# Kernel tuning notes

Measured on AMD Instinct MI355X. Metric: run time of the kernel, lower is better.

## Reference

```python
import jax, jax.numpy as jnp
import numpy as np

B_, L_, H_, D_, N_, R_, K_ = 2, 1024, 2048, 4096, 16, 128, 4


def setup_inputs() -> dict:
    key = jax.random.key(0)
    ks = jax.random.split(key, 8)
    s = lambda k, shp, sc: jax.random.normal(k, shp, jnp.float32) * sc
    x = s(ks[0], (B_, L_, H_), 1.0)
    in_proj_w = s(ks[1], (2 * D_, H_), 0.02)
    conv_w = s(ks[2], (D_, 1, K_), 0.1)          # depthwise conv kernel (OIW, I=1)
    conv_b = s(ks[3], (D_,), 0.02)
    x_proj_w = s(ks[4], (R_ + 2 * N_, D_), 0.02)
    dt_proj_w = s(ks[5], (D_, R_), 0.02)
    dt_proj_b = s(ks[6], (D_,), 0.02)
    # A_log init as in module: log(arange(1..N)) expanded over channels
    A_log = jnp.log(jnp.broadcast_to(jnp.arange(1, N_ + 1, dtype=jnp.float32), (D_, N_)))
    D = jnp.ones((D_,), jnp.float32)
    out_proj_w = s(ks[7], (H_, D_), 0.02)
    return dict(x=x, in_proj_w=in_proj_w, conv_w=conv_w, conv_b=conv_b,
                x_proj_w=x_proj_w, dt_proj_w=dt_proj_w, dt_proj_b=dt_proj_b,
                A_log=A_log, D=D, out_proj_w=out_proj_w)


def reference(x, in_proj_w, conv_w, conv_b, x_proj_w, dt_proj_w, dt_proj_b, A_log, D, out_proj_w):
    Bsz, L, H = x.shape
    # in_proj -> split into ssm branch and gate branch
    proj = x @ in_proj_w.T                               # [B, L, 2D]
    h, gate = jnp.split(proj, 2, axis=-1)                # each [B, L, D]
    # causal depthwise conv1d over time (left pad K-1, truncate to L)
    hc = h.transpose(0, 2, 1)                            # [B, D, L]
    conv = jax.lax.conv_general_dilated(
        hc, conv_w, window_strides=(1,), padding=[(K_ - 1, 0)],
        dimension_numbers=('NCW', 'OIW', 'NCW'), feature_group_count=hc.shape[1])
    u = jax.nn.silu(conv + conv_b[None, :, None]).transpose(0, 2, 1)  # [B, L, D]
    # input-dependent SSM parameters
    ssm_p = u @ x_proj_w.T                               # [B, L, R+2N]
    dt, Bm, Cm = jnp.split(ssm_p, [R_, R_ + N_], axis=-1)
    dt = jax.nn.softplus(dt @ dt_proj_w.T + dt_proj_b)   # [B, L, D]
    A = -jnp.exp(A_log)                                  # [D, N]

    def step(state, inp):
        dt_t, B_t, C_t, u_t = inp                        # [B,D],[B,N],[B,N],[B,D]
        dA = jnp.exp(dt_t[:, :, None] * A)               # [B, D, N]
        dBu = dt_t[:, :, None] * B_t[:, None, :] * u_t[:, :, None]
        state = state * dA + dBu                         # [B, D, N]
        y = jnp.einsum('bdn,bn->bd', state, C_t)
        return state, y

    init = jnp.zeros((Bsz, u.shape[-1], N_), x.dtype)
    _, ys = jax.lax.scan(step, init, (dt.transpose(1, 0, 2), Bm.transpose(1, 0, 2),
                                      Cm.transpose(1, 0, 2), u.transpose(1, 0, 2)))
    y = ys.transpose(1, 0, 2)                            # [B, L, D]
    y = (y + u * D) * jax.nn.silu(gate)
    return y @ out_proj_w.T                              # [B, L, H]
```

## Files before the change

### kernel.cpp

```cpp
#include <hip/hip_runtime.h>
#include <hip/hip_bf16.h>
#include <cstdint>
#include <cstddef>

typedef __hip_bfloat16 bf16;
typedef __attribute__((ext_vector_type(8))) short short8;
typedef __attribute__((ext_vector_type(4))) float f32x4;

#define BB 2
#define LL 1024
#define HH 2048
#define DD 4096
#define NN 16
#define RR 128
#define KK 4
#define TT (BB*LL)
#define NC 16
#define LC (LL/NC)
#define KSPLIT 8

__device__ __forceinline__ void gload_lds16(const void* g, void* l) {
  __builtin_amdgcn_global_load_lds(
      (__attribute__((address_space(1))) void*)(g),
      (__attribute__((address_space(3))) void*)(l), 16, 0, 0);
}

__global__ void probe_dtype(const unsigned int* __restrict__ alog, int* __restrict__ flag) {
  if (threadIdx.x == 0 && blockIdx.x == 0) *flag = (alog[0] != 0u) ? 1 : 0;
}

__global__ __launch_bounds__(256) void cvt_bf16(
    const void* __restrict__ src, bf16* __restrict__ dst,
    int n4, const int* __restrict__ flag)
{
  const bool isb = (*flag != 0);
  const int stride = gridDim.x * blockDim.x;
  for (int i = blockIdx.x * blockDim.x + threadIdx.x; i < n4; i += stride) {
    if (isb) {
      ((uint2*)dst)[i] = ((const uint2*)src)[i];
    } else {
      float4 v = ((const float4*)src)[i];
      dst[i*4+0] = __float2bfloat16(v.x);
      dst[i*4+1] = __float2bfloat16(v.y);
      dst[i*4+2] = __float2bfloat16(v.z);
      dst[i*4+3] = __float2bfloat16(v.w);
    }
  }
}

template<int EPI>
__global__ __launch_bounds__(512, 1) void gemm256(
    const bf16* __restrict__ A, const bf16* __restrict__ Bw,
    bf16* __restrict__ Cb, float* __restrict__ Cf,
    int M, int N, int K, int ldk)
{
  __shared__ __align__(16) short As[2*256*64];
  __shared__ __align__(16) short Bs[2*256*64];
  const int tid = threadIdx.x;
  const int w = tid >> 6, l = tid & 63;
  const int lr = l & 15, lk = l >> 4;
  const int wr = w >> 2, wc = w & 3;
  const int m0 = blockIdx.x * 256, n0 = blockIdx.y * 256;

  const int nt = K >> 6;

  const int srow = w*8 + (l>>3);
  const int scol = (((l&7) ^ (l>>3)) << 3);
  const int sld  = srow*64 + (l&7)*8;

  f32x4 acc[8][4] = {};

  const bf16* Ab = A  + (size_t)m0 * ldk;
  const bf16* Bb = Bw + (size_t)n0 * ldk;

  auto stage = [&](int t) {
    const int buf = (t & 1) * 16384;
    const size_t kk = (size_t)(t << 6);
#pragma unroll
    for (int i = 0; i < 4; i++)
      gload_lds16(Ab + (size_t)(i*64 + srow) * ldk + kk + scol, &As[buf + i*4096 + sld]);
#pragma unroll
    for (int i = 0; i < 4; i++)
      gload_lds16(Bb + (size_t)(i*64 + srow) * ldk + kk + scol, &Bs[buf + i*4096 + sld]);
  };

  stage(0);
  stage(1);
  asm volatile("s_waitcnt vmcnt(8)" ::: "memory");
  __builtin_amdgcn_s_barrier();

  for (int t = 0; t < nt; ++t) {
    const int buf = (t & 1) * 16384;
    short8 bfr[4][2];
#pragma unroll
    for (int nf = 0; nf < 4; nf++) {
      const int r = wc*64 + nf*16 + lr;
#pragma unroll
      for (int ks = 0; ks < 2; ks++)
        bfr[nf][ks] = *(const short8*)&Bs[buf + r*64 + (((ks*4+lk) ^ (r&7)) << 3)];
    }
#pragma unroll
    for (int q = 0; q < 4; q++) {
      short8 afr[2][2];
#pragma unroll
      for (int mi = 0; mi < 2; mi++) {
        const int r = wr*128 + (q*2+mi)*16 + lr;
#pragma unroll
        for (int ks = 0; ks < 2; ks++)
          afr[mi][ks] = *(const short8*)&As[buf + r*64 + (((ks*4+lk) ^ (r&7)) << 3)];
      }
#pragma unroll
      for (int mi = 0; mi < 2; mi++)
#pragma unroll
        for (int nf = 0; nf < 4; nf++)
#pragma unroll
          for (int ks = 0; ks < 2; ks++)
            acc[q*2+mi][nf] = __builtin_amdgcn_mfma_f32_16x16x32_bf16(
                afr[mi][ks], bfr[nf][ks], acc[q*2+mi][nf], 0, 0, 0);
    }
    if (t + 1 < nt) {
      asm volatile("" ::: "memory");
      __builtin_amdgcn_s_barrier();
      if (t + 2 < nt) {
        stage(t + 2);
        asm volatile("s_waitcnt vmcnt(8)" ::: "memory");
      } else {
        asm volatile("s_waitcnt vmcnt(0)" ::: "memory");
      }
      __builtin_amdgcn_s_barrier();
    }
  }

#pragma unroll
  for (int mf = 0; mf < 8; mf++)
#pragma unroll
    for (int nf = 0; nf < 4; nf++)
#pragma unroll
      for (int r = 0; r < 4; r++) {
        const int row = m0 + wr*128 + mf*16 + lk*4 + r;
        const int col = n0 + wc*64 + nf*16 + lr;
        const float v = acc[mf][nf][r];
        if constexpr (EPI == 0) {
          Cb[(size_t)row*N + col] = __float2bfloat16(v);
        } else {
          Cf[(size_t)blockIdx.z*M*N + (size_t)row*N + col] = v;
        }
      }
}

__global__ __launch_bounds__(256) void reduce_out(
    const float* __restrict__ part, bf16* __restrict__ ob, float* __restrict__ of,
    const int* __restrict__ flag)
{
  const int id = blockIdx.x*256 + threadIdx.x;
  const bool isb = (*flag != 0);
  float4 a = ((const float4*)part)[id];
  const float4 b = ((const float4*)(part + (size_t)TT*HH))[id];
  a.x += b.x; a.y += b.y; a.z += b.z; a.w += b.w;
  if (isb) {
    ob[id*4+0] = __float2bfloat16(a.x);
    ob[id*4+1] = __float2bfloat16(a.y);
    ob[id*4+2] = __float2bfloat16(a.z);
    ob[id*4+3] = __float2bfloat16(a.w);
  } else {
    ((float4*)of)[id] = a;
  }
}

template<int EPI>
__global__ __launch_bounds__(256) void gemm_bt(
    const bf16* __restrict__ A, const bf16* __restrict__ Bw,
    bf16* __restrict__ Cb, float* __restrict__ Cf,
    const void* __restrict__ bias,
    int M, int N, int K, int ldk, int Nvalid, const int* __restrict__ flag)
{
  __shared__ __align__(16) short As[3*128*32];
  __shared__ __align__(16) short Bs[3*128*32];
  const int tid = threadIdx.x;
  const int w = tid >> 6, l = tid & 63;
  const int lr = l & 15, lk = l >> 4;
  const int m0 = blockIdx.x * 128, n0 = blockIdx.y * 128;
  const int wm = (w >> 1) * 64, wn = (w & 1) * 64;

  f32x4 acc[4][4] = {};

  const int sr0 = (w*2+0)*16 + (l>>2);
  const int sr1 = (w*2+1)*16 + (l>>2);
  const int sc0 = (((l&3) ^ ((sr0>>1)&3)) << 3);
  const int sc1 = (((l&3) ^ ((sr1>>1)&3)) << 3);
  const int lo0 = (w*2+0)*512 + l*8;
  const int lo1 = (w*2+1)*512 + l*8;

  const size_t arow0 = (size_t)(m0 + sr0);
  const size_t arow1 = (size_t)(m0 + sr1);
  const size_t brow0 = (size_t)min(n0 + sr0, N-1);
  const size_t brow1 = (size_t)min(n0 + sr1, N-1);
  const size_t kb = (size_t)blockIdx.z * K;

  const int NT = K >> 5;

  auto stage = [&](int t) {
    const int s = t % 3;
    const size_t ko = kb + (size_t)(t << 5);
    gload_lds16(A  + arow0*ldk + ko + sc0, &As[s*4096 + lo0]);
    gload_lds16(A  + arow1*ldk + ko + sc1, &As[s*4096 + lo1]);
    gload_lds16(Bw + brow0*ldk + ko + sc0, &Bs[s*4096 + lo0]);
    gload_lds16(Bw + brow1*ldk + ko + sc1, &Bs[s*4096 + lo1]);
  };

  stage(0);
  stage(1);
  asm volatile("s_waitcnt vmcnt(4)" ::: "memory");
  __builtin_amdgcn_s_barrier();

  for (int t = 0; t < NT; ++t) {
    if (t + 2 < NT) stage(t + 2);
    const int s = t % 3;
    short8 a[4], b[4];
#pragma unroll
    for (int m = 0; m < 4; m++) {
      const int row = wm + m*16 + lr;
      a[m] = *(const short8*)&As[s*4096 + row*32 + ((lk ^ ((row>>1)&3)) << 3)];
    }
#pragma unroll
    for (int n = 0; n < 4; n++) {
      const int row = wn + n*16 + lr;
      b[n] = *(const short8*)&Bs[s*4096 + row*32 + ((lk ^ ((row>>1)&3)) << 3)];
    }
#pragma unroll
    for (int m = 0; m < 4; m++)
#pragma unroll
      for (int n = 0; n < 4; n++)
        acc[m][n] = __builtin_amdgcn_mfma_f32_16x16x32_bf16(a[m], b[n], acc[m][n], 0, 0, 0);

    if (t + 2 < NT) {
      asm volatile("s_waitcnt vmcnt(4)" ::: "memory");
      __builtin_amdgcn_s_barrier();
    } else if (t + 1 < NT) {
      asm volatile("s_waitcnt vmcnt(0)" ::: "memory");
      __builtin_amdgcn_s_barrier();
    }
  }

  bool isb = false;
  if constexpr (EPI == 1) isb = (*flag != 0);

#pragma unroll
  for (int m = 0; m < 4; m++) {
#pragma unroll
    for (int n = 0; n < 4; n++) {
#pragma unroll
      for (int r = 0; r < 4; r++) {
        const int row = m0 + wm + m*16 + lk*4 + r;
        const int col = n0 + wn + n*16 + lr;
        float v = acc[m][n][r];
        if constexpr (EPI == 1) {
          const float bv = isb ? __bfloat162float(((const bf16*)bias)[col])
                               : ((const float*)bias)[col];
          v += bv;
          v = fmaxf(v, 0.f) + log1pf(expf(-fabsf(v)));
          Cb[(size_t)row*N + col] = __float2bfloat16(v);
        } else {
          if (col < Nvalid)
            Cf[(size_t)blockIdx.z*M*Nvalid + (size_t)row*Nvalid + col] = v;
        }
      }
    }
  }
}

__global__ __launch_bounds__(256) void reduce_ssm(
    const float* __restrict__ part, float* __restrict__ ssm,
    bf16* __restrict__ dtin)
{
  const int id = blockIdx.x*256 + threadIdx.x;
  const int row = id / 160, col = id - row*160;
  float v = 0.f;
#pragma unroll
  for (int s = 0; s < KSPLIT; s++) v += part[(size_t)s*TT*160 + id];
  ssm[id] = v;
  if (col < 128) dtin[(size_t)row*128 + col] = __float2bfloat16(v);
}

__global__ __launch_bounds__(256) void conv_silu(
    const bf16* __restrict__ proj, const void* __restrict__ cw,
    const void* __restrict__ cb, bf16* __restrict__ u,
    const int* __restrict__ flag)
{
  const int d  = blockIdx.x * 256 + threadIdx.x;
  const int t0 = blockIdx.y * 64;
  const int l0 = t0 & (LL-1);
  const bool isb = (*flag != 0);
  float w0, w1, w2, w3, bv;
  if (isb) {
    const bf16* c = (const bf16*)cw;
    w0 = __bfloat162float(c[d*KK+0]); w1 = __bfloat162float(c[d*KK+1]);
    w2 = __bfloat162float(c[d*KK+2]); w3 = __bfloat162float(c[d*KK+3]);
    bv = __bfloat162float(((const bf16*)cb)[d]);
  } else {
    const float* c = (const float*)cw;
    w0 = c[d*KK+0]; w1 = c[d*KK+1]; w2 = c[d*KK+2]; w3 = c[d*KK+3];
    bv = ((const float*)cb)[d];
  }
  float hm3 = 0.f, hm2 = 0.f, hm1 = 0.f;
  if (l0 > 0) {
    hm3 = __bfloat162float(proj[(size_t)(t0-3)*(2*DD) + d]);
    hm2 = __bfloat162float(proj[(size_t)(t0-2)*(2*DD) + d]);
    hm1 = __bfloat162float(proj[(size_t)(t0-1)*(2*DD) + d]);
  }
  for (int i = 0; i < 64; i++) {
    const int t = t0 + i;
    const float hc = __bfloat162float(proj[(size_t)t*(2*DD) + d]);
    const float a = bv + w0*hm3 + w1*hm2 + w2*hm1 + w3*hc;
    const float s = a / (1.f + __expf(-a));
    u[(size_t)t*DD + d] = __float2bfloat16(s);
    hm3 = hm2; hm2 = hm1; hm1 = hc;
  }
}

__global__ __launch_bounds__(256) void scan_pass1(
    const bf16* __restrict__ dt, const bf16* __restrict__ u,
    const float* __restrict__ ssm, const void* __restrict__ Alog,
    float* __restrict__ dtsum, float* __restrict__ Sb,
    const int* __restrict__ flag)
{
  const int d = blockIdx.x * 256 + threadIdx.x;
  const int c = blockIdx.y, b = blockIdx.z;
  const bool isb = (*flag != 0);
  float Av[NN];
#pragma unroll
  for (int n = 0; n < NN; n++) {
    const float alv = isb ? __bfloat162float(((const bf16*)Alog)[d*NN + n])
                          : ((const float*)Alog)[d*NN + n];
    Av[n] = -__expf(alv);
  }
  float st[NN];
#pragma unroll
  for (int n = 0; n < NN; n++) st[n] = 0.f;
  float dsum = 0.f;
  const size_t tok0 = (size_t)b * LL + (size_t)c * LC;

  float dtv = __bfloat162float(dt[tok0*DD + d]);
  float uv  = __bfloat162float(u [tok0*DD + d]);
  float4 Bp0 = *(const float4*)&ssm[tok0*160 + RR];
  float4 Bp1 = *(const float4*)&ssm[tok0*160 + RR + 4];
  float4 Bp2 = *(const float4*)&ssm[tok0*160 + RR + 8];
  float4 Bp3 = *(const float4*)&ssm[tok0*160 + RR + 12];

  for (int i = 0; i < LC; i++) {
    const float dtc = dtv, uc = uv;
    const float Bv[NN] = {Bp0.x,Bp0.y,Bp0.z,Bp0.w, Bp1.x,Bp1.y,Bp1.z,Bp1.w,
                          Bp2.x,Bp2.y,Bp2.z,Bp2.w, Bp3.x,Bp3.y,Bp3.z,Bp3.w};
    if (i < LC-1) {
      const size_t tk = tok0 + i + 1;
      dtv = __bfloat162float(dt[tk*DD + d]);
      uv  = __bfloat162float(u [tk*DD + d]);
      Bp0 = *(const float4*)&ssm[tk*160 + RR];
      Bp1 = *(const float4*)&ssm[tk*160 + RR + 4];
      Bp2 = *(const float4*)&ssm[tk*160 + RR + 8];
      Bp3 = *(const float4*)&ssm[tk*160 + RR + 12];
    }
    const float dtu = dtc * uc;
    dsum += dtc;
#pragma unroll
    for (int n = 0; n < NN; n++) {
      const float dA = __expf(dtc * Av[n]);
      st[n] = fmaf(st[n], dA, Bv[n] * dtu);
    }
  }
  dtsum[((size_t)b*NC + c)*DD + d] = dsum;
  float4* Sp = (float4*)&Sb[(((size_t)b*NC + c)*DD + d)*NN];
  Sp[0] = make_float4(st[0],  st[1],  st[2],  st[3]);
  Sp[1] = make_float4(st[4],  st[5],  st[6],  st[7]);
  Sp[2] = make_float4(st[8],  st[9],  st[10], st[11]);
  Sp[3] = make_float4(st[12], st[13], st[14], st[15]);
}

__global__ __launch_bounds__(256) void scan_pass2(
    const float* __restrict__ dtsum, float* __restrict__ Sb,
    const void* __restrict__ Alog, const int* __restrict__ flag)
{
  const int id = blockIdx.x * 256 + threadIdx.x;
  const int b = id >> 16;
  const int r = id & (DD*NN - 1);
  const int d = r >> 4, n = r & 15;
  const bool isb = (*flag != 0);
  const float alv = isb ? __bfloat162float(((const bf16*)Alog)[d*NN + n])
                        : ((const float*)Alog)[d*NN + n];
  const float Av = -__expf(alv);
  float carry = 0.f;
  size_t sidx = (size_t)b * NC * DD * NN + r;
  size_t didx = (size_t)b * NC * DD + d;
#pragma unroll
  for (int c = 0; c < NC; c++) {
    const float p = __expf(Av * dtsum[didx]);
    const float s = Sb[sidx];
    Sb[sidx] = carry;
    carry = p * carry + s;
    sidx += (size_t)DD * NN;
    didx += (size_t)DD;
  }
}

__global__ __launch_bounds__(256) void scan_pass3(
    const bf16* __restrict__ dt, const bf16* __restrict__ u,
    const float* __restrict__ ssm, const bf16* __restrict__ proj,
    const void* __restrict__ Alog, const void* __restrict__ Dp,
    const float* __restrict__ Sb,
    bf16* __restrict__ yout, const int* __restrict__ flag)
{
  const int d = blockIdx.x * 256 + threadIdx.x;
  const int c = blockIdx.y, b = blockIdx.z;
  const bool isb = (*flag != 0);
  float Av[NN];
#pragma unroll
  for (int n = 0; n < NN; n++) {
    const float alv = isb ? __bfloat162float(((const bf16*)Alog)[d*NN + n])
                          : ((const float*)Alog)[d*NN + n];
    Av[n] = -__expf(alv);
  }
  const float Dval = isb ? __bfloat162float(((const bf16*)Dp)[d])
                         : ((const float*)Dp)[d];
  float st[NN];
  {
    const float4* Sp = (const float4*)&Sb[(((size_t)b*NC + c)*DD + d)*NN];
    float4 s0 = Sp[0], s1 = Sp[1], s2 = Sp[2], s3 = Sp[3];
    st[0]=s0.x; st[1]=s0.y; st[2]=s0.z; st[3]=s0.w;
    st[4]=s1.x; st[5]=s1.y; st[6]=s1.z; st[7]=s1.w;
    st[8]=s2.x; st[9]=s2.y; st[10]=s2.z; st[11]=s2.w;
    st[12]=s3.x; st[13]=s3.y; st[14]=s3.z; st[15]=s3.w;
  }
  const size_t tok0 = (size_t)b * LL + (size_t)c * LC;

  float dtv = __bfloat162float(dt[tok0*DD + d]);
  float uv  = __bfloat162float(u [tok0*DD + d]);
  float gv  = __bfloat162float(proj[tok0*(2*DD) + DD + d]);
  float4 Bp0 = *(const float4*)&ssm[tok0*160 + RR];
  float4 Bp1 = *(const float4*)&ssm[tok0*160 + RR + 4];
  float4 Bp2 = *(const float4*)&ssm[tok0*160 + RR + 8];
  float4 Bp3 = *(const float4*)&ssm[tok0*160 + RR + 12];
  float4 Cp0 = *(const float4*)&ssm[tok0*160 + RR + NN];
  float4 Cp1 = *(const float4*)&ssm[tok0*160 + RR + NN + 4];
  float4 Cp2 = *(const float4*)&ssm[tok0*160 + RR + NN + 8];
  float4 Cp3 = *(const float4*)&ssm[tok0*160 + RR + NN + 12];

  for (int i = 0; i < LC; i++) {
    const float dtc = dtv, uc = uv, gc = gv;
    const float Bv[NN] = {Bp0.x,Bp0.y,Bp0.z,Bp0.w, Bp1.x,Bp1.y,Bp1.z,Bp1.w,
                          Bp2.x,Bp2.y,Bp2.z,Bp2.w, Bp3.x,Bp3.y,Bp3.z,Bp3.w};
    const float Cv[NN] = {Cp0.x,Cp0.y,Cp0.z,Cp0.w, Cp1.x,Cp1.y,Cp1.z,Cp1.w,
                          Cp2.x,Cp2.y,Cp2.z,Cp2.w, Cp3.x,Cp3.y,Cp3.z,Cp3.w};
    if (i < LC-1) {
      const size_t tk = tok0 + i + 1;
      dtv = __bfloat162float(dt[tk*DD + d]);
      uv  = __bfloat162float(u [tk*DD + d]);
      gv  = __bfloat162float(proj[tk*(2*DD) + DD + d]);
      Bp0 = *(const float4*)&ssm[tk*160 + RR];
      Bp1 = *(const float4*)&ssm[tk*160 + RR + 4];
      Bp2 = *(const float4*)&ssm[tk*160 + RR + 8];
      Bp3 = *(const float4*)&ssm[tk*160 + RR + 12];
      Cp0 = *(const float4*)&ssm[tk*160 + RR + NN];
      Cp1 = *(const float4*)&ssm[tk*160 + RR + NN + 4];
      Cp2 = *(const float4*)&ssm[tk*160 + RR + NN + 8];
      Cp3 = *(const float4*)&ssm[tk*160 + RR + NN + 12];
    }
    const float dtu = dtc * uc;
    float y = uc * Dval;
#pragma unroll
    for (int n = 0; n < NN; n++) {
      const float dA = __expf(dtc * Av[n]);
      st[n] = fmaf(st[n], dA, Bv[n] * dtu);
      y = fmaf(st[n], Cv[n], y);
    }
    const float sg = gc / (1.f + __expf(-gc));
    yout[(tok0 + i)*DD + d] = __float2bfloat16(y * sg);
  }
}

extern "C" void kernel_launch(void* const* d_in, const int* in_sizes, int n_in,
                              void* d_out, int out_size, void* d_ws, size_t ws_size,
                              hipStream_t stream)
{
  const void* x    = d_in[0];
  const void* wIn  = d_in[1];
  const void* cw   = d_in[2];
  const void* cb   = d_in[3];
  const void* xw   = d_in[4];
  const void* dtw  = d_in[5];
  const void* dtb  = d_in[6];
  const void* Alog = d_in[7];
  const void* Dp   = d_in[8];
  const void* ow   = d_in[9];

  char* ws = (char*)d_ws;
  bf16*  proj  = (bf16*) (ws + 0);
  bf16*  u     = (bf16*) (ws + 33554432);
  float* ssm   = (float*)(ws + 50331648);
  bf16*  dtin  = (bf16*) (ws + 51642368);
  bf16*  dtbuf = (bf16*) (ws + 52166656);
  bf16*  yfin  = (bf16*) (ws + 68943872);
  bf16*  xb    = (bf16*) (ws + 52166656);
  bf16*  wInb  = (bf16*) (ws + 60555264);
  float* part  = (float*)(ws + 52166656);
  bf16*  owb   = (bf16*) (ws + 52166656);
  float* part6 = (float*)(ws + 0);
  float* dtsum = (float*)(ws + 51642368);
  float* Sbuf  = (float*)(ws + 85721088);
  bf16*  xwb   = (bf16*) (ws + 94109696);
  bf16*  dtwb  = (bf16*) (ws + 95420416);
  int*   flag  = (int*)  (ws + 96468992);

  probe_dtype<<<1, 64, 0, stream>>>((const unsigned int*)Alog, flag);
  cvt_bf16<<<1024, 256, 0, stream>>>(x,   xb,   (BB*LL*HH)/4,   flag);
  cvt_bf16<<<1024, 256, 0, stream>>>(wIn, wInb, (2*DD*HH)/4,    flag);
  cvt_bf16<<<256,  256, 0, stream>>>(xw,  xwb,  ((RR+2*NN)*DD)/4, flag);
  cvt_bf16<<<256,  256, 0, stream>>>(dtw, dtwb, (DD*RR)/4,      flag);

  gemm256<0><<<dim3(TT/256, (2*DD)/256), 512, 0, stream>>>(
      xb, wInb, proj, nullptr, TT, 2*DD, HH, HH);
  conv_silu<<<dim3(DD/256, TT/64), 256, 0, stream>>>(proj, cw, cb, u, flag);
  gemm_bt<4><<<dim3(TT/128, 2, KSPLIT), 256, 0, stream>>>(
      u, xwb, nullptr, part, nullptr, TT, RR + 2*NN, DD/KSPLIT, DD, RR + 2*NN, flag);
  reduce_ssm<<<dim3(TT*160/256), 256, 0, stream>>>(part, ssm, dtin);
  gemm_bt<1><<<dim3(TT/128, DD/128), 256, 0, stream>>>(
      dtin, dtwb, dtbuf, nullptr, dtb, TT, DD, RR, RR, DD, flag);
  scan_pass1<<<dim3(DD/256, NC, BB), 256, 0, stream>>>(
      dtbuf, u, ssm, Alog, dtsum, Sbuf, flag);
  scan_pass2<<<dim3(BB*DD*NN/256), 256, 0, stream>>>(dtsum, Sbuf, Alog, flag);
  scan_pass3<<<dim3(DD/256, NC, BB), 256, 0, stream>>>(
      dtbuf, u, ssm, proj, Alog, Dp, Sbuf, yfin, flag);
  cvt_bf16<<<1024, 256, 0, stream>>>(ow, owb, (HH*DD)/4, flag);
  gemm_bt<4><<<dim3(TT/128, HH/128, 2), 256, 0, stream>>>(
      yfin, owb, nullptr, part6, nullptr, TT, HH, DD/2, DD, HH, flag);
  reduce_out<<<dim3(TT*HH/4/256), 256, 0, stream>>>(
      part6, (bf16*)d_out, (float*)d_out, flag);
}
```

Baseline: 325.5 us.

## Split SSM state across thread pairs in scan kernels and pack bf16 stores

The chunked scan pass1 and pass3 kernels now give each channel to two threads, each holding 8 of the 16 state elements. This doubles the grid and halves per-thread registers and serial work. Pass3 combines the partial y with a lane shuffle. Separately, the bf16 conversion and output-reduce kernels write packed 8-byte stores instead of four scalar bf16 stores, and gemm256 drops its unused fp32 epilogue branch. The cost is duplicated dt/u/gate loads and an extra shuffle per timestep.

```diff
diff --git a/kernel.cpp b/kernel.cpp
--- a/kernel.cpp
+++ b/kernel.cpp
@@ -25,6 +25,12 @@
       (__attribute__((address_space(3))) void*)(l), 16, 0, 0);
 }
 
+__device__ __forceinline__ unsigned int pk2bf(float a, float b) {
+  union { bf16 h; unsigned short u; } ua, ub;
+  ua.h = __float2bfloat16(a); ub.h = __float2bfloat16(b);
+  return (unsigned int)ua.u | ((unsigned int)ub.u << 16);
+}
+
 __global__ void probe_dtype(const unsigned int* __restrict__ alog, int* __restrict__ flag) {
   if (threadIdx.x == 0 && blockIdx.x == 0) *flag = (alog[0] != 0u) ? 1 : 0;
 }
@@ -40,10 +46,7 @@
       ((uint2*)dst)[i] = ((const uint2*)src)[i];
     } else {
       float4 v = ((const float4*)src)[i];
-      dst[i*4+0] = __float2bfloat16(v.x);
-      dst[i*4+1] = __float2bfloat16(v.y);
-      dst[i*4+2] = __float2bfloat16(v.z);
-      dst[i*4+3] = __float2bfloat16(v.w);
+      ((uint2*)dst)[i] = make_uint2(pk2bf(v.x, v.y), pk2bf(v.z, v.w));
     }
   }
 }
@@ -139,12 +142,7 @@
       for (int r = 0; r < 4; r++) {
         const int row = m0 + wr*128 + mf*16 + lk*4 + r;
         const int col = n0 + wc*64 + nf*16 + lr;
-        const float v = acc[mf][nf][r];
-        if constexpr (EPI == 0) {
-          Cb[(size_t)row*N + col] = __float2bfloat16(v);
-        } else {
-          Cf[(size_t)blockIdx.z*M*N + (size_t)row*N + col] = v;
-        }
+        Cb[(size_t)row*N + col] = __float2bfloat16(acc[mf][nf][r]);
       }
 }
 
@@ -158,10 +156,7 @@
   const float4 b = ((const float4*)(part + (size_t)TT*HH))[id];
   a.x += b.x; a.y += b.y; a.z += b.z; a.w += b.w;
   if (isb) {
-    ob[id*4+0] = __float2bfloat16(a.x);
-    ob[id*4+1] = __float2bfloat16(a.y);
-    ob[id*4+2] = __float2bfloat16(a.z);
-    ob[id*4+3] = __float2bfloat16(a.w);
+    ((uint2*)ob)[id] = make_uint2(pk2bf(a.x, a.y), pk2bf(a.z, a.w));
   } else {
     ((float4*)of)[id] = a;
   }
@@ -324,56 +319,52 @@
     float* __restrict__ dtsum, float* __restrict__ Sb,
     const int* __restrict__ flag)
 {
-  const int d = blockIdx.x * 256 + threadIdx.x;
+  const int tid = threadIdx.x;
+  const int h = tid & 1;
+  const int d = blockIdx.x * 128 + (tid >> 1);
   const int c = blockIdx.y, b = blockIdx.z;
   const bool isb = (*flag != 0);
-  float Av[NN];
-#pragma unroll
-  for (int n = 0; n < NN; n++) {
-    const float alv = isb ? __bfloat162float(((const bf16*)Alog)[d*NN + n])
-                          : ((const float*)Alog)[d*NN + n];
+  const int nb = h * 8;
+  float Av[8];
+#pragma unroll
+  for (int n = 0; n < 8; n++) {
+    const float alv = isb ? __bfloat162float(((const bf16*)Alog)[d*NN + nb + n])
+                          : ((const float*)Alog)[d*NN + nb + n];
     Av[n] = -__expf(alv);
   }
-  float st[NN];
-#pragma unroll
-  for (int n = 0; n < NN; n++) st[n] = 0.f;
+  float st[8];
+#pragma unroll
+  for (int n = 0; n < 8; n++) st[n] = 0.f;
   float dsum = 0.f;
   const size_t tok0 = (size_t)b * LL + (size_t)c * LC;
 
   float dtv = __bfloat162float(dt[tok0*DD + d]);
   float uv  = __bfloat162float(u [tok0*DD + d]);
-  float4 Bp0 = *(const float4*)&ssm[tok0*160 + RR];
-  float4 Bp1 = *(const float4*)&ssm[tok0*160 + RR + 4];
-  float4 Bp2 = *(const float4*)&ssm[tok0*160 + RR + 8];
-  float4 Bp3 = *(const float4*)&ssm[tok0*160 + RR + 12];
+  float4 Bp0 = *(const float4*)&ssm[tok0*160 + RR + nb];
+  float4 Bp1 = *(const float4*)&ssm[tok0*160 + RR + nb + 4];
 
   for (int i = 0; i < LC; i++) {
     const float dtc = dtv, uc = uv;
-    const float Bv[NN] = {Bp0.x,Bp0.y,Bp0.z,Bp0.w, Bp1.x,Bp1.y,Bp1.z,Bp1.w,
-                          Bp2.x,Bp2.y,Bp2.z,Bp2.w, Bp3.x,Bp3.y,Bp3.z,Bp3.w};
+    const float Bv[8] = {Bp0.x,Bp0.y,Bp0.z,Bp0.w, Bp1.x,Bp1.y,Bp1.z,Bp1.w};
     if (i < LC-1) {
       const size_t tk = tok0 + i + 1;
       dtv = __bfloat162float(dt[tk*DD + d]);
       uv  = __bfloat162float(u [tk*DD + d]);
-      Bp0 = *(const float4*)&ssm[tk*160 + RR];
-      Bp1 = *(const float4*)&ssm[tk*160 + RR + 4];
-      Bp2 = *(const float4*)&ssm[tk*160 + RR + 8];
-      Bp3 = *(const float4*)&ssm[tk*160 + RR + 12];
+      Bp0 = *(const float4*)&ssm[tk*160 + RR + nb];
+      Bp1 = *(const float4*)&ssm[tk*160 + RR + nb + 4];
     }
     const float dtu = dtc * uc;
     dsum += dtc;
 #pragma unroll
-    for (int n = 0; n < NN; n++) {
+    for (int n = 0; n < 8; n++) {
       const float dA = __expf(dtc * Av[n]);
       st[n] = fmaf(st[n], dA, Bv[n] * dtu);
     }
   }
-  dtsum[((size_t)b*NC + c)*DD + d] = dsum;
+  if (h == 0) dtsum[((size_t)b*NC + c)*DD + d] = dsum;
   float4* Sp = (float4*)&Sb[(((size_t)b*NC + c)*DD + d)*NN];
-  Sp[0] = make_float4(st[0],  st[1],  st[2],  st[3]);
-  Sp[1] = make_float4(st[4],  st[5],  st[6],  st[7]);
-  Sp[2] = make_float4(st[8],  st[9],  st[10], st[11]);
-  Sp[3] = make_float4(st[12], st[13], st[14], st[15]);
+  Sp[h*2+0] = make_float4(st[0], st[1], st[2], st[3]);
+  Sp[h*2+1] = make_float4(st[4], st[5], st[6], st[7]);
 }
 
 __global__ __launch_bounds__(256) void scan_pass2(
@@ -409,71 +400,65 @@
     const float* __restrict__ Sb,
     bf16* __restrict__ yout, const int* __restrict__ flag)
 {
-  const int d = blockIdx.x * 256 + threadIdx.x;
+  const int tid = threadIdx.x;
+  const int h = tid & 1;
+  const int d = blockIdx.x * 128 + (tid >> 1);
   const int c = blockIdx.y, b = blockIdx.z;
   const bool isb = (*flag != 0);
-  float Av[NN];
-#pragma unroll
-  for (int n = 0; n < NN; n++) {
-    const float alv = isb ? __bfloat162float(((const bf16*)Alog)[d*NN + n])
-                          : ((const float*)Alog)[d*NN + n];
+  const int nb = h * 8;
+  float Av[8];
+#pragma unroll
+  for (int n = 0; n < 8; n++) {
+    const float alv = isb ? __bfloat162float(((const bf16*)Alog)[d*NN + nb + n])
+                          : ((const float*)Alog)[d*NN + nb + n];
     Av[n] = -__expf(alv);
   }
   const float Dval = isb ? __bfloat162float(((const bf16*)Dp)[d])
                          : ((const float*)Dp)[d];
-  float st[NN];
+  float st[8];
   {
     const float4* Sp = (const float4*)&Sb[(((size_t)b*NC + c)*DD + d)*NN];
-    float4 s0 = Sp[0], s1 = Sp[1], s2 = Sp[2], s3 = Sp[3];
+    float4 s0 = Sp[h*2+0], s1 = Sp[h*2+1];
     st[0]=s0.x; st[1]=s0.y; st[2]=s0.z; st[3]=s0.w;
     st[4]=s1.x; st[5]=s1.y; st[6]=s1.z; st[7]=s1.w;
-    st[8]=s2.x; st[9]=s2.y; st[10]=s2.z; st[11]=s2.w;
-    st[12]=s3.x; st[13]=s3.y; st[14]=s3.z; st[15]=s3.w;
   }
   const size_t tok0 = (size_t)b * LL + (size_t)c * LC;
 
   float dtv = __bfloat162float(dt[tok0*DD + d]);
   float uv  = __bfloat162float(u [tok0*DD + d]);
   float gv  = __bfloat162float(proj[tok0*(2*DD) + DD + d]);
-  float4 Bp0 = *(const float4*)&ssm[tok0*160 + RR];
-  float4 Bp1 = *(const float4*)&ssm[tok0*160 + RR + 4];
-  float4 Bp2 = *(const float4*)&ssm[tok0*160 + RR + 8];
-  float4 Bp3 = *(const float4*)&ssm[tok0*160 + RR + 12];
-  float4 Cp0 = *(const float4*)&ssm[tok0*160 + RR + NN];
-  float4 Cp1 = *(const float4*)&ssm[tok0*160 + RR + NN + 4];
-  float4 Cp2 = *(const float4*)&ssm[tok0*160 + RR + NN + 8];
-  float4 Cp3 = *(const float4*)&ssm[tok0*160 + RR + NN + 12];
+  float4 Bp0 = *(const float4*)&ssm[tok0*160 + RR + nb];
+  float4 Bp1 = *(const float4*)&ssm[tok0*160 + RR + nb + 4];
+  float4 Cp0 = *(const float4*)&ssm[tok0*160 + RR + NN + nb];
+  float4 Cp1 = *(const float4*)&ssm[tok0*160 + RR + NN + nb + 4];
 
   for (int i = 0; i < LC; i++) {
     const float dtc = dtv, uc = uv, gc = gv;
-    const float Bv[NN] = {Bp0.x,Bp0.y,Bp0.z,Bp0.w, Bp1.x,Bp1.y,Bp1.z,Bp1.w,
-                          Bp2.x,Bp2.y,Bp2.z,Bp2.w, Bp3.x,Bp3.y,Bp3.z,Bp3.w};
-    const float Cv[NN] = {Cp0.x,Cp0.y,Cp0.z,Cp0.w, Cp1.x,Cp1.y,Cp1.z,Cp1.w,
-                          Cp2.x,Cp2.y,Cp2.z,Cp2.w, Cp3.x,Cp3.y,Cp3.z,Cp3.w};
+    const float Bv[8] = {Bp0.x,Bp0.y,Bp0.z,Bp0.w, Bp1.x,Bp1.y,Bp1.z,Bp1.w};
+    const float Cv[8] = {Cp0.x,Cp0.y,Cp0.z,Cp0.w, Cp1.x,Cp1.y,Cp1.z,Cp1.w};
     if (i < LC-1) {
       const size_t tk = tok0 + i + 1;
       dtv = __bfloat162float(dt[tk*DD + d]);
       uv  = __bfloat162float(u [tk*DD + d]);
       gv  = __bfloat162float(proj[tk*(2*DD) + DD + d]);
-      Bp0 = *(const float4*)&ssm[tk*160 + RR];
-      Bp1 = *(const float4*)&ssm[tk*160 + RR + 4];
-      Bp2 = *(const float4*)&ssm[tk*160 + RR + 8];
-      Bp3 = *(const float4*)&ssm[tk*160 + RR + 12];
-      Cp0 = *(const float4*)&ssm[tk*160 + RR + NN];
-      Cp1 = *(const float4*)&ssm[tk*160 + RR + NN + 4];
-      Cp2 = *(const float4*)&ssm[tk*160 + RR + NN + 8];
-      Cp3 = *(const float4*)&ssm[tk*160 + RR + NN + 12];
+      Bp0 = *(const float4*)&ssm[tk*160 + RR + nb];
+      Bp1 = *(const float4*)&ssm[tk*160 + RR + nb + 4];
+      Cp0 = *(const float4*)&ssm[tk*160 + RR + NN + nb];
+      Cp1 = *(const float4*)&ssm[tk*160 + RR + NN + nb + 4];
     }
     const float dtu = dtc * uc;
-    float y = uc * Dval;
-#pragma unroll
-    for (int n = 0; n < NN; n++) {
+    float y = (h == 0) ? uc * Dval : 0.f;
+#pragma unroll
+    for (int n = 0; n < 8; n++) {
       const float dA = __expf(dtc * Av[n]);
       st[n] = fmaf(st[n], dA, Bv[n] * dtu);
       y = fmaf(st[n], Cv[n], y);
     }
-    const float sg = gc / (1.f + __expf(-gc));
-    yout[(tok0 + i)*DD + d] = __float2bfloat16(y * sg);
+    y += __shfl_xor(y, 1);
+    if (h == 0) {
+      const float sg = gc / (1.f + __expf(-gc));
+      yout[(tok0 + i)*DD + d] = __float2bfloat16(y * sg);
+    }
   }
 }
 
@@ -524,10 +509,10 @@
   reduce_ssm<<<dim3(TT*160/256), 256, 0, stream>>>(part, ssm, dtin);
   gemm_bt<1><<<dim3(TT/128, DD/128), 256, 0, stream>>>(
       dtin, dtwb, dtbuf, nullptr, dtb, TT, DD, RR, RR, DD, flag);
-  scan_pass1<<<dim3(DD/256, NC, BB), 256, 0, stream>>>(
+  scan_pass1<<<dim3(DD/128, NC, BB), 256, 0, stream>>>(
       dtbuf, u, ssm, Alog, dtsum, Sbuf, flag);
   scan_pass2<<<dim3(BB*DD*NN/256), 256, 0, stream>>>(dtsum, Sbuf, Alog, flag);
-  scan_pass3<<<dim3(DD/256, NC, BB), 256, 0, stream>>>(
+  scan_pass3<<<dim3(DD/128, NC, BB), 256, 0, stream>>>(
       dtbuf, u, ssm, proj, Alog, Dp, Sbuf, yfin, flag);
   cvt_bf16<<<1024, 256, 0, stream>>>(ow, owb, (HH*DD)/4, flag);
   gemm_bt<4><<<dim3(TT/128, HH/128, 2), 256, 0, stream>>>(
```

After: 336.0 us. +3.2%, slower.
